# Kernel tuning notes

Hardware: AMD Instinct MI355X
Metric: run time of the kernel (lower is better)

## Reference

```python
import jax, jax.numpy as jnp
import numpy as np

B = 65536
D = 8          # model dim (hard-wired in source)
H = 2          # num_heads
A = 20         # act_size
L = 5          # tokens per embedding stream


def _attn_layer(x, Wqkv, bqkv, Wo, bo, Wl, bl):
    # x: [B, S, D]
    Bx, S, Dx = x.shape
    hd = Dx // H
    qkv = x @ Wqkv.T + bqkv                      # [B, S, 3D]
    q, k, v = jnp.split(qkv, 3, axis=-1)
    def split_heads(t):
        return t.reshape(Bx, S, H, hd).transpose(0, 2, 1, 3)  # [B,H,S,hd]
    q, k, v = split_heads(q), split_heads(k), split_heads(v)
    scores = jnp.einsum('bhqd,bhkd->bhqk', q, k) * (hd ** -0.5)
    attn = jax.nn.softmax(scores, axis=-1)       # dropout inactive at eval
    o = jnp.einsum('bhqk,bhkd->bhqd', attn, v)
    o = o.transpose(0, 2, 1, 3).reshape(Bx, S, Dx)
    x = x + (o @ Wo.T + bo)                      # residual after attention
    h = jax.nn.relu(x @ Wl.T + bl)               # linear + relu
    return x + h                                 # second residual


def setup_inputs() -> dict:
    key = jax.random.key(0)
    ks = jax.random.split(key, 20)
    s = 1.0 / np.sqrt(D)
    inp = {
        'dice_type': jax.random.randint(ks[0], (B, L), 0, 15),
        'dice_star': jax.random.randint(ks[1], (B, L), 0, 15),
        'summon_lvl': jax.random.randint(ks[2], (B, L), 0, 2),
        'emb_dice': jax.random.normal(ks[3], (15, D), jnp.float32),
        'emb_star': jax.random.normal(ks[4], (15, D), jnp.float32),
        'emb_btns': jax.random.normal(ks[5], (2, D), jnp.float32),
        'Wout': jax.random.normal(ks[6], (A, D), jnp.float32) * s,
        'bout': jnp.zeros((A,), jnp.float32),
    }
    for i in range(2):
        o = 7 + 5 * i
        inp[f'Wqkv{i}'] = jax.random.normal(ks[o], (3 * D, D), jnp.float32) * s
        inp[f'bqkv{i}'] = jnp.zeros((3 * D,), jnp.float32)
        inp[f'Wo{i}'] = jax.random.normal(ks[o + 1], (D, D), jnp.float32) * s
        inp[f'bo{i}'] = jnp.zeros((D,), jnp.float32)
        inp[f'Wl{i}'] = jax.random.normal(ks[o + 2], (D, D), jnp.float32) * s
        inp[f'bl{i}'] = jnp.zeros((D,), jnp.float32)
    return inp


def reference(dice_type, dice_star, summon_lvl,
              emb_dice, emb_star, emb_btns,
              Wqkv0, bqkv0, Wo0, bo0, Wl0, bl0,
              Wqkv1, bqkv1, Wo1, bo1, Wl1, bl1,
              Wout, bout):
    x = jnp.concatenate([emb_dice[dice_type],
                         emb_star[dice_star],
                         emb_btns[summon_lvl]], axis=1)  # [B, 15, D]
    x = _attn_layer(x, Wqkv0, bqkv0, Wo0, bo0, Wl0, bl0)
    x = _attn_layer(x, Wqkv1, bqkv1, Wo1, bo1, Wl1, bl1)
    x = jnp.mean(x, axis=1)                               # [B, D]
    return x @ Wout.T + bout                              # [B, A]
```

## Files before the change

kernel.cpp:

```cpp
#include <hip/hip_runtime.h>
#include <math.h>

#define EPB 16
#define BTOT 65536
#define C_SCALE 0.72134752044f
#define QSTR 28

__device__ __forceinline__ float exp2_fast(float x) {
#if defined(__has_builtin)
#if __has_builtin(__builtin_amdgcn_exp2f)
  return __builtin_amdgcn_exp2f(x);
#else
  return exp2f(x);
#endif
#else
  return exp2f(x);
#endif
}

__global__ __launch_bounds__(256) void BetterBot_44169443672375_kernel(
    const int* __restrict__ dice_type, const int* __restrict__ dice_star,
    const int* __restrict__ summon_lvl,
    const float* __restrict__ emb_dice, const float* __restrict__ emb_star,
    const float* __restrict__ emb_btns,
    const float* __restrict__ Wout, const float* __restrict__ bout,
    const float* __restrict__ Wqkv0, const float* __restrict__ bqkv0,
    const float* __restrict__ Wo0, const float* __restrict__ bo0,
    const float* __restrict__ Wl0, const float* __restrict__ bl0,
    const float* __restrict__ Wqkv1, const float* __restrict__ bqkv1,
    const float* __restrict__ Wo1, const float* __restrict__ bo1,
    const float* __restrict__ Wl1, const float* __restrict__ bl1,
    float* __restrict__ out)
{
  __shared__ __align__(16) float qkvT[32 * QSTR];
  __shared__ __align__(8)  float2 eT[32 * 33];
  __shared__ __align__(16) float xT[32][8];
  __shared__ int idxT[EPB][17];
  __shared__ __align__(16) float kb[EPB][17][8];
  __shared__ __align__(16) float vb[EPB][17][8];

  const int tid = threadIdx.x;
  const int e = tid >> 4;
  const int t = tid & 15;
  const int ge = blockIdx.x * EPB + e;

  int myc = 0;
  if (t < 15) {
    int c;
    if (t < 5)       c = dice_type[ge * 5 + t];
    else if (t < 10) c = 15 + dice_star[ge * 5 + (t - 5)];
    else             c = 30 + summon_lvl[ge * 5 + (t - 10)];
    idxT[e][t] = c;
    myc = c;
  }
  {
    const int c = tid >> 3;
    const int l8 = tid & 7;
    const float* er;
    if (c < 15)      er = emb_dice + 8 * c;
    else if (c < 30) er = emb_star + 8 * (c - 15);
    else             er = emb_btns + 8 * (c - 30);
    const float4 r0 = ((const float4*)er)[0];
    const float4 r1 = ((const float4*)er)[1];
    float r[8] = {r0.x, r0.y, r0.z, r0.w, r1.x, r1.y, r1.z, r1.w};
    xT[c][l8] = r[l8];
#pragma unroll
    for (int cc = 0; cc < 3; ++cc) {
      const int col = l8 * 3 + cc;
      float acc = bqkv0[col];
#pragma unroll
      for (int j = 0; j < 8; ++j) acc = fmaf(r[j], Wqkv0[col * 8 + j], acc);
      qkvT[c * QSTR + col] = acc;
    }
  }
  __syncthreads();

  {
    const int p0 = tid * 4;
    const int qi = p0 >> 5;
    const float* qr = qkvT + qi * QSTR;
    float qv[8];
#pragma unroll
    for (int j = 0; j < 8; ++j) qv[j] = qr[j];
#pragma unroll
    for (int jj = 0; jj < 4; ++jj) {
      const int ki = (p0 & 31) + jj;
      const float* kr = qkvT + ki * QSTR + 8;
      float s0 = qv[0] * kr[0];
      s0 = fmaf(qv[1], kr[1], s0); s0 = fmaf(qv[2], kr[2], s0); s0 = fmaf(qv[3], kr[3], s0);
      float s1 = qv[4] * kr[4];
      s1 = fmaf(qv[5], kr[5], s1); s1 = fmaf(qv[6], kr[6], s1); s1 = fmaf(qv[7], kr[7], s1);
      eT[qi * 33 + ki] = make_float2(exp2_fast(C_SCALE * s0), exp2_fast(C_SCALE * s1));
    }
  }
  __syncthreads();

  float x[8] = {0.f, 0.f, 0.f, 0.f, 0.f, 0.f, 0.f, 0.f};
  float q1[8];
  if (t < 15) {
    const float4 x0a = *(const float4*)(xT[myc]);
    const float4 x0b = *(const float4*)(xT[myc] + 4);
    x[0] = x0a.x; x[1] = x0a.y; x[2] = x0a.z; x[3] = x0a.w;
    x[4] = x0b.x; x[5] = x0b.y; x[6] = x0b.z; x[7] = x0b.w;

    float o[8] = {0.f, 0.f, 0.f, 0.f, 0.f, 0.f, 0.f, 0.f};
    float sum0 = 0.f, sum1 = 0.f;
    const float2* myE = eT + myc * 33;
#pragma unroll
    for (int u = 0; u < 15; ++u) {
      const int uc = idxT[e][u];
      const float2 ee = myE[uc];
      const float4 v0 = *(const float4*)(qkvT + uc * QSTR + 16);
      const float4 v1 = *(const float4*)(qkvT + uc * QSTR + 20);
      sum0 += ee.x; sum1 += ee.y;
      o[0] = fmaf(ee.x, v0.x, o[0]); o[1] = fmaf(ee.x, v0.y, o[1]);
      o[2] = fmaf(ee.x, v0.z, o[2]); o[3] = fmaf(ee.x, v0.w, o[3]);
      o[4] = fmaf(ee.y, v1.x, o[4]); o[5] = fmaf(ee.y, v1.y, o[5]);
      o[6] = fmaf(ee.y, v1.z, o[6]); o[7] = fmaf(ee.y, v1.w, o[7]);
    }
    const float r0 = 1.0f / sum0, r1 = 1.0f / sum1;
#pragma unroll
    for (int d = 0; d < 4; ++d) { o[d] *= r0; o[4 + d] *= r1; }
    float xn[8];
#pragma unroll
    for (int c = 0; c < 8; ++c) {
      float acc = bo0[c];
#pragma unroll
      for (int j = 0; j < 8; ++j) acc = fmaf(o[j], Wo0[c * 8 + j], acc);
      xn[c] = x[c] + acc;
    }
#pragma unroll
    for (int c = 0; c < 8; ++c) {
      float acc = bl0[c];
#pragma unroll
      for (int j = 0; j < 8; ++j) acc = fmaf(xn[j], Wl0[c * 8 + j], acc);
      x[c] = xn[c] + fmaxf(acc, 0.0f);
    }

    float k1[8], v1[8];
#pragma unroll
    for (int c = 0; c < 8; ++c) {
      float aq = bqkv1[c];
      float ak = bqkv1[8 + c];
      float av = bqkv1[16 + c];
#pragma unroll
      for (int j = 0; j < 8; ++j) {
        aq = fmaf(x[j], Wqkv1[c * 8 + j], aq);
        ak = fmaf(x[j], Wqkv1[(8 + c) * 8 + j], ak);
        av = fmaf(x[j], Wqkv1[(16 + c) * 8 + j], av);
      }
      q1[c] = aq * C_SCALE;
      k1[c] = ak; v1[c] = av;
    }
    float4* kd = (float4*)kb[e][t];
    kd[0] = make_float4(k1[0], k1[1], k1[2], k1[3]);
    kd[1] = make_float4(k1[4], k1[5], k1[6], k1[7]);
    float4* vd = (float4*)vb[e][t];
    vd[0] = make_float4(v1[0], v1[1], v1[2], v1[3]);
    vd[1] = make_float4(v1[4], v1[5], v1[6], v1[7]);
  }
  __syncthreads();

  if (t < 15) {
    float o[8] = {0.f, 0.f, 0.f, 0.f, 0.f, 0.f, 0.f, 0.f};
    float sum0 = 0.f, sum1 = 0.f;
#pragma unroll
    for (int u = 0; u < 15; ++u) {
      const float4 k0 = *(const float4*)(kb[e][u]);
      const float4 k1v = *(const float4*)(kb[e][u] + 4);
      const float4 v0 = *(const float4*)(vb[e][u]);
      const float4 v1 = *(const float4*)(vb[e][u] + 4);
      float s0 = q1[0] * k0.x;
      s0 = fmaf(q1[1], k0.y, s0); s0 = fmaf(q1[2], k0.z, s0); s0 = fmaf(q1[3], k0.w, s0);
      float s1 = q1[4] * k1v.x;
      s1 = fmaf(q1[5], k1v.y, s1); s1 = fmaf(q1[6], k1v.z, s1); s1 = fmaf(q1[7], k1v.w, s1);
      const float e0 = exp2_fast(s0);
      const float e1 = exp2_fast(s1);
      sum0 += e0; sum1 += e1;
      o[0] = fmaf(e0, v0.x, o[0]); o[1] = fmaf(e0, v0.y, o[1]);
      o[2] = fmaf(e0, v0.z, o[2]); o[3] = fmaf(e0, v0.w, o[3]);
      o[4] = fmaf(e1, v1.x, o[4]); o[5] = fmaf(e1, v1.y, o[5]);
      o[6] = fmaf(e1, v1.z, o[6]); o[7] = fmaf(e1, v1.w, o[7]);
    }
    const float r0 = 1.0f / sum0, r1 = 1.0f / sum1;
#pragma unroll
    for (int d = 0; d < 4; ++d) { o[d] *= r0; o[4 + d] *= r1; }
    float xn[8];
#pragma unroll
    for (int c = 0; c < 8; ++c) {
      float acc = bo1[c];
#pragma unroll
      for (int j = 0; j < 8; ++j) acc = fmaf(o[j], Wo1[c * 8 + j], acc);
      xn[c] = x[c] + acc;
    }
#pragma unroll
    for (int c = 0; c < 8; ++c) {
      float acc = bl1[c];
#pragma unroll
      for (int j = 0; j < 8; ++j) acc = fmaf(xn[j], Wl1[c * 8 + j], acc);
      x[c] = xn[c] + fmaxf(acc, 0.0f);
    }
  }

  float p[8];
#pragma unroll
  for (int j = 0; j < 8; ++j) p[j] = x[j];
#pragma unroll
  for (int j = 0; j < 8; ++j) p[j] += __shfl_xor(p[j], 1);
#pragma unroll
  for (int j = 0; j < 8; ++j) p[j] += __shfl_xor(p[j], 2);
#pragma unroll
  for (int j = 0; j < 8; ++j) p[j] += __shfl_xor(p[j], 4);
#pragma unroll
  for (int j = 0; j < 8; ++j) p[j] += __shfl_xor(p[j], 8);
  float mean[8];
#pragma unroll
  for (int j = 0; j < 8; ++j) mean[j] = p[j] * (1.0f / 15.0f);

  const int obase = ge * 20;
  {
    float acc = bout[t];
#pragma unroll
    for (int j = 0; j < 8; ++j) acc = fmaf(mean[j], Wout[t * 8 + j], acc);
    out[obase + t] = acc;
  }
  if (t < 4) {
    const int a = 16 + t;
    float acc = bout[a];
#pragma unroll
    for (int j = 0; j < 8; ++j) acc = fmaf(mean[j], Wout[a * 8 + j], acc);
    out[obase + a] = acc;
  }
}

extern "C" void kernel_launch(void* const* d_in, const int* in_sizes, int n_in,
                              void* d_out, int out_size, void* d_ws, size_t ws_size,
                              hipStream_t stream) {
  const int*   dice_type  = (const int*)d_in[0];
  const int*   dice_star  = (const int*)d_in[1];
  const int*   summon_lvl = (const int*)d_in[2];
  const float* emb_dice   = (const float*)d_in[3];
  const float* emb_star   = (const float*)d_in[4];
  const float* emb_btns   = (const float*)d_in[5];
  const float* Wout       = (const float*)d_in[6];
  const float* bout       = (const float*)d_in[7];
  const float* Wqkv0      = (const float*)d_in[8];
  const float* bqkv0      = (const float*)d_in[9];
  const float* Wo0        = (const float*)d_in[10];
  const float* bo0        = (const float*)d_in[11];
  const float* Wl0        = (const float*)d_in[12];
  const float* bl0        = (const float*)d_in[13];
  const float* Wqkv1      = (const float*)d_in[14];
  const float* bqkv1      = (const float*)d_in[15];
  const float* Wo1        = (const float*)d_in[16];
  const float* bo1        = (const float*)d_in[17];
  const float* Wl1        = (const float*)d_in[18];
  const float* bl1        = (const float*)d_in[19];
  float* out = (float*)d_out;

  dim3 grid(BTOT / EPB), block(256);
  hipLaunchKernelGGL(BetterBot_44169443672375_kernel, grid, block, 0, stream,
                     dice_type, dice_star, summon_lvl,
                     emb_dice, emb_star, emb_btns, Wout, bout,
                     Wqkv0, bqkv0, Wo0, bo0, Wl0, bl0,
                     Wqkv1, bqkv1, Wo1, bo1, Wl1, bl1,
                     out);
}
```

Baseline: 128.7 us.

## Move layer-0 attention output and small matmuls to packed fp16 math

Adds a setup kernel that packs the small weight matrices into fp16 pairs, with the query scale folded in, and stores them in workspace. The main kernel then runs the layer-0 attention accumulation, the output and linear projections, and the layer-1 QKV projection with packed half2 arithmetic. Shared buffers are shrunk and merged, and a launch-bounds occupancy hint is added. The aim is to halve ALU instruction count and cut LDS footprint. The cost is fp16 rounding error in the residual stream and one extra small kernel launch per call.

```diff
diff --git a/kernel.cpp b/kernel.cpp
--- a/kernel.cpp
+++ b/kernel.cpp
@@ -4,7 +4,19 @@
 #define EPB 16
 #define BTOT 65536
 #define C_SCALE 0.72134752044f
-#define QSTR 28
+
+typedef _Float16 h2 __attribute__((ext_vector_type(2)));
+
+#define WQKV1 0
+#define BQKV1 96
+#define WO0   108
+#define BO0   140
+#define WL0   144
+#define BL0   176
+#define WO1   180
+#define BO1   212
+#define WL1   216
+#define BL1   248
 
 __device__ __forceinline__ float exp2_fast(float x) {
 #if defined(__has_builtin)
@@ -18,26 +30,84 @@
 #endif
 }
 
-__global__ __launch_bounds__(256) void BetterBot_44169443672375_kernel(
+union F4H2 { float4 f; h2 h[4]; };
+
+__device__ __forceinline__ void mm8_h2(const h2* __restrict__ wp, int woff, int boff,
+                                       const h2 in2[4], h2 out2[4])
+{
+#pragma unroll
+  for (int c2 = 0; c2 < 4; ++c2) {
+    h2 acc = wp[boff + c2];
+#pragma unroll
+    for (int p = 0; p < 4; ++p) {
+      acc += (h2)(in2[p].x) * wp[woff + c2 * 8 + 2 * p];
+      acc += (h2)(in2[p].y) * wp[woff + c2 * 8 + 2 * p + 1];
+    }
+    out2[c2] = acc;
+  }
+}
+
+__global__ void BetterBot_setup(const float* __restrict__ Wqkv1, const float* __restrict__ bqkv1,
+                                const float* __restrict__ Wo0, const float* __restrict__ bo0,
+                                const float* __restrict__ Wl0, const float* __restrict__ bl0,
+                                const float* __restrict__ Wo1, const float* __restrict__ bo1,
+                                const float* __restrict__ Wl1, const float* __restrict__ bl1,
+                                h2* __restrict__ ws)
+{
+  const int tid = threadIdx.x;
+  if (tid < 96) {
+    const int c2 = tid >> 3, j = tid & 7;
+    float a = Wqkv1[(2 * c2) * 8 + j], b = Wqkv1[(2 * c2 + 1) * 8 + j];
+    if (c2 < 4) { a *= C_SCALE; b *= C_SCALE; }
+    ws[tid] = (h2){(_Float16)a, (_Float16)b};
+  } else if (tid < 108) {
+    const int c2 = tid - 96;
+    float a = bqkv1[2 * c2], b = bqkv1[2 * c2 + 1];
+    if (c2 < 4) { a *= C_SCALE; b *= C_SCALE; }
+    ws[tid] = (h2){(_Float16)a, (_Float16)b};
+  } else if (tid < 140) {
+    const int k = tid - 108, c2 = k >> 3, j = k & 7;
+    ws[tid] = (h2){(_Float16)Wo0[(2 * c2) * 8 + j], (_Float16)Wo0[(2 * c2 + 1) * 8 + j]};
+  } else if (tid < 144) {
+    const int c2 = tid - 140;
+    ws[tid] = (h2){(_Float16)bo0[2 * c2], (_Float16)bo0[2 * c2 + 1]};
+  } else if (tid < 176) {
+    const int k = tid - 144, c2 = k >> 3, j = k & 7;
+    ws[tid] = (h2){(_Float16)Wl0[(2 * c2) * 8 + j], (_Float16)Wl0[(2 * c2 + 1) * 8 + j]};
+  } else if (tid < 180) {
+    const int c2 = tid - 176;
+    ws[tid] = (h2){(_Float16)bl0[2 * c2], (_Float16)bl0[2 * c2 + 1]};
+  } else if (tid < 212) {
+    const int k = tid - 180, c2 = k >> 3, j = k & 7;
+    ws[tid] = (h2){(_Float16)Wo1[(2 * c2) * 8 + j], (_Float16)Wo1[(2 * c2 + 1) * 8 + j]};
+  } else if (tid < 216) {
+    const int c2 = tid - 212;
+    ws[tid] = (h2){(_Float16)bo1[2 * c2], (_Float16)bo1[2 * c2 + 1]};
+  } else if (tid < 248) {
+    const int k = tid - 216, c2 = k >> 3, j = k & 7;
+    ws[tid] = (h2){(_Float16)Wl1[(2 * c2) * 8 + j], (_Float16)Wl1[(2 * c2 + 1) * 8 + j]};
+  } else if (tid < 252) {
+    const int c2 = tid - 248;
+    ws[tid] = (h2){(_Float16)bl1[2 * c2], (_Float16)bl1[2 * c2 + 1]};
+  }
+}
+
+__global__ __launch_bounds__(256, 4) void BetterBot_44169443672375_kernel(
     const int* __restrict__ dice_type, const int* __restrict__ dice_star,
     const int* __restrict__ summon_lvl,
     const float* __restrict__ emb_dice, const float* __restrict__ emb_star,
     const float* __restrict__ emb_btns,
     const float* __restrict__ Wout, const float* __restrict__ bout,
     const float* __restrict__ Wqkv0, const float* __restrict__ bqkv0,
-    const float* __restrict__ Wo0, const float* __restrict__ bo0,
-    const float* __restrict__ Wl0, const float* __restrict__ bl0,
-    const float* __restrict__ Wqkv1, const float* __restrict__ bqkv1,
-    const float* __restrict__ Wo1, const float* __restrict__ bo1,
-    const float* __restrict__ Wl1, const float* __restrict__ bl1,
+    const h2* __restrict__ wp,
     float* __restrict__ out)
 {
-  __shared__ __align__(16) float qkvT[32 * QSTR];
-  __shared__ __align__(8)  float2 eT[32 * 33];
-  __shared__ __align__(16) float xT[32][8];
-  __shared__ int idxT[EPB][17];
-  __shared__ __align__(16) float kb[EPB][17][8];
-  __shared__ __align__(16) float vb[EPB][17][8];
+  __shared__ __align__(16) float qkT[32][20];
+  __shared__ __align__(16) h2 vT[32][4];
+  __shared__ __align__(16) h2 xT[32][4];
+  __shared__ h2 eT[32 * 33];
+  __shared__ int idxT[EPB][16];
+  __shared__ __align__(16) float kvb[EPB][15][16];
 
   const int tid = threadIdx.x;
   const int e = tid >> 4;
@@ -63,148 +133,150 @@
     const float4 r0 = ((const float4*)er)[0];
     const float4 r1 = ((const float4*)er)[1];
     float r[8] = {r0.x, r0.y, r0.z, r0.w, r1.x, r1.y, r1.z, r1.w};
-    xT[c][l8] = r[l8];
-#pragma unroll
-    for (int cc = 0; cc < 3; ++cc) {
-      const int col = l8 * 3 + cc;
-      float acc = bqkv0[col];
-#pragma unroll
-      for (int j = 0; j < 8; ++j) acc = fmaf(r[j], Wqkv0[col * 8 + j], acc);
-      qkvT[c * QSTR + col] = acc;
-    }
+    if (l8 < 4) xT[c][l8] = (h2){(_Float16)r[2 * l8], (_Float16)r[2 * l8 + 1]};
+    float aq = bqkv0[l8], ak = bqkv0[8 + l8], av = bqkv0[16 + l8];
+#pragma unroll
+    for (int j = 0; j < 8; ++j) {
+      aq = fmaf(r[j], Wqkv0[l8 * 8 + j], aq);
+      ak = fmaf(r[j], Wqkv0[(8 + l8) * 8 + j], ak);
+      av = fmaf(r[j], Wqkv0[(16 + l8) * 8 + j], av);
+    }
+    qkT[c][l8] = aq * C_SCALE;
+    qkT[c][8 + l8] = ak;
+    const float vn = __shfl_xor(av, 1);
+    if ((l8 & 1) == 0) vT[c][l8 >> 1] = (h2){(_Float16)av, (_Float16)vn};
   }
   __syncthreads();
 
   {
-    const int p0 = tid * 4;
-    const int qi = p0 >> 5;
-    const float* qr = qkvT + qi * QSTR;
+    const int qi = tid >> 3;
+    const int ki0 = (tid & 7) * 4;
     float qv[8];
 #pragma unroll
-    for (int j = 0; j < 8; ++j) qv[j] = qr[j];
+    for (int j = 0; j < 8; ++j) qv[j] = qkT[qi][j];
 #pragma unroll
     for (int jj = 0; jj < 4; ++jj) {
-      const int ki = (p0 & 31) + jj;
-      const float* kr = qkvT + ki * QSTR + 8;
+      const int ki = ki0 + jj;
+      const float* kr = &qkT[ki][8];
       float s0 = qv[0] * kr[0];
       s0 = fmaf(qv[1], kr[1], s0); s0 = fmaf(qv[2], kr[2], s0); s0 = fmaf(qv[3], kr[3], s0);
       float s1 = qv[4] * kr[4];
       s1 = fmaf(qv[5], kr[5], s1); s1 = fmaf(qv[6], kr[6], s1); s1 = fmaf(qv[7], kr[7], s1);
-      eT[qi * 33 + ki] = make_float2(exp2_fast(C_SCALE * s0), exp2_fast(C_SCALE * s1));
+      eT[qi * 33 + ki] = (h2){(_Float16)exp2_fast(s0), (_Float16)exp2_fast(s1)};
     }
   }
   __syncthreads();
 
-  float x[8] = {0.f, 0.f, 0.f, 0.f, 0.f, 0.f, 0.f, 0.f};
-  float q1[8];
+  h2 x2[4];
+  float q1f[8];
   if (t < 15) {
-    const float4 x0a = *(const float4*)(xT[myc]);
-    const float4 x0b = *(const float4*)(xT[myc] + 4);
-    x[0] = x0a.x; x[1] = x0a.y; x[2] = x0a.z; x[3] = x0a.w;
-    x[4] = x0b.x; x[5] = x0b.y; x[6] = x0b.z; x[7] = x0b.w;
-
-    float o[8] = {0.f, 0.f, 0.f, 0.f, 0.f, 0.f, 0.f, 0.f};
+    F4H2 xx; xx.f = *(const float4*)(&xT[myc][0]);
+#pragma unroll
+    for (int p = 0; p < 4; ++p) x2[p] = xx.h[p];
+
+    h2 o2[4] = {(h2)(_Float16)0.f, (h2)(_Float16)0.f, (h2)(_Float16)0.f, (h2)(_Float16)0.f};
     float sum0 = 0.f, sum1 = 0.f;
-    const float2* myE = eT + myc * 33;
+    const h2* myE = eT + myc * 33;
 #pragma unroll
     for (int u = 0; u < 15; ++u) {
       const int uc = idxT[e][u];
-      const float2 ee = myE[uc];
-      const float4 v0 = *(const float4*)(qkvT + uc * QSTR + 16);
-      const float4 v1 = *(const float4*)(qkvT + uc * QSTR + 20);
-      sum0 += ee.x; sum1 += ee.y;
-      o[0] = fmaf(ee.x, v0.x, o[0]); o[1] = fmaf(ee.x, v0.y, o[1]);
-      o[2] = fmaf(ee.x, v0.z, o[2]); o[3] = fmaf(ee.x, v0.w, o[3]);
-      o[4] = fmaf(ee.y, v1.x, o[4]); o[5] = fmaf(ee.y, v1.y, o[5]);
-      o[6] = fmaf(ee.y, v1.z, o[6]); o[7] = fmaf(ee.y, v1.w, o[7]);
+      const h2 ee = myE[uc];
+      F4H2 vv; vv.f = *(const float4*)(&vT[uc][0]);
+      const h2 el = (h2)(ee.x);
+      const h2 eh = (h2)(ee.y);
+      o2[0] += el * vv.h[0];
+      o2[1] += el * vv.h[1];
+      o2[2] += eh * vv.h[2];
+      o2[3] += eh * vv.h[3];
+      sum0 += (float)ee.x;
+      sum1 += (float)ee.y;
     }
     const float r0 = 1.0f / sum0, r1 = 1.0f / sum1;
-#pragma unroll
-    for (int d = 0; d < 4; ++d) { o[d] *= r0; o[4 + d] *= r1; }
-    float xn[8];
-#pragma unroll
-    for (int c = 0; c < 8; ++c) {
-      float acc = bo0[c];
-#pragma unroll
-      for (int j = 0; j < 8; ++j) acc = fmaf(o[j], Wo0[c * 8 + j], acc);
-      xn[c] = x[c] + acc;
-    }
-#pragma unroll
-    for (int c = 0; c < 8; ++c) {
-      float acc = bl0[c];
-#pragma unroll
-      for (int j = 0; j < 8; ++j) acc = fmaf(xn[j], Wl0[c * 8 + j], acc);
-      x[c] = xn[c] + fmaxf(acc, 0.0f);
-    }
-
-    float k1[8], v1[8];
-#pragma unroll
-    for (int c = 0; c < 8; ++c) {
-      float aq = bqkv1[c];
-      float ak = bqkv1[8 + c];
-      float av = bqkv1[16 + c];
-#pragma unroll
-      for (int j = 0; j < 8; ++j) {
-        aq = fmaf(x[j], Wqkv1[c * 8 + j], aq);
-        ak = fmaf(x[j], Wqkv1[(8 + c) * 8 + j], ak);
-        av = fmaf(x[j], Wqkv1[(16 + c) * 8 + j], av);
+    o2[0] *= (h2)(_Float16)r0; o2[1] *= (h2)(_Float16)r0;
+    o2[2] *= (h2)(_Float16)r1; o2[3] *= (h2)(_Float16)r1;
+
+    h2 y2[4], xn2[4], hh2[4];
+    mm8_h2(wp, WO0, BO0, o2, y2);
+#pragma unroll
+    for (int p = 0; p < 4; ++p) xn2[p] = x2[p] + y2[p];
+    mm8_h2(wp, WL0, BL0, xn2, hh2);
+    const h2 z2 = (h2)(_Float16)0.f;
+#pragma unroll
+    for (int p = 0; p < 4; ++p) x2[p] = xn2[p] + __builtin_elementwise_max(hh2[p], z2);
+
+    h2 qkv2[12];
+#pragma unroll
+    for (int c2 = 0; c2 < 12; ++c2) {
+      h2 acc = wp[BQKV1 + c2];
+#pragma unroll
+      for (int p = 0; p < 4; ++p) {
+        acc += (h2)(x2[p].x) * wp[WQKV1 + c2 * 8 + 2 * p];
+        acc += (h2)(x2[p].y) * wp[WQKV1 + c2 * 8 + 2 * p + 1];
       }
-      q1[c] = aq * C_SCALE;
-      k1[c] = ak; v1[c] = av;
-    }
-    float4* kd = (float4*)kb[e][t];
-    kd[0] = make_float4(k1[0], k1[1], k1[2], k1[3]);
-    kd[1] = make_float4(k1[4], k1[5], k1[6], k1[7]);
-    float4* vd = (float4*)vb[e][t];
-    vd[0] = make_float4(v1[0], v1[1], v1[2], v1[3]);
-    vd[1] = make_float4(v1[4], v1[5], v1[6], v1[7]);
+      qkv2[c2] = acc;
+    }
+#pragma unroll
+    for (int p = 0; p < 4; ++p) {
+      q1f[2 * p] = (float)qkv2[p].x;
+      q1f[2 * p + 1] = (float)qkv2[p].y;
+    }
+    *(float4*)(&kvb[e][t][0]) = make_float4((float)qkv2[4].x, (float)qkv2[4].y,
+                                            (float)qkv2[5].x, (float)qkv2[5].y);
+    *(float4*)(&kvb[e][t][4]) = make_float4((float)qkv2[6].x, (float)qkv2[6].y,
+                                            (float)qkv2[7].x, (float)qkv2[7].y);
+    *(float4*)(&kvb[e][t][8]) = make_float4((float)qkv2[8].x, (float)qkv2[8].y,
+                                            (float)qkv2[9].x, (float)qkv2[9].y);
+    *(float4*)(&kvb[e][t][12]) = make_float4((float)qkv2[10].x, (float)qkv2[10].y,
+                                             (float)qkv2[11].x, (float)qkv2[11].y);
   }
   __syncthreads();
 
+  float xo[8] = {0.f, 0.f, 0.f, 0.f, 0.f, 0.f, 0.f, 0.f};
   if (t < 15) {
     float o[8] = {0.f, 0.f, 0.f, 0.f, 0.f, 0.f, 0.f, 0.f};
     float sum0 = 0.f, sum1 = 0.f;
 #pragma unroll
     for (int u = 0; u < 15; ++u) {
-      const float4 k0 = *(const float4*)(kb[e][u]);
-      const float4 k1v = *(const float4*)(kb[e][u] + 4);
-      const float4 v0 = *(const float4*)(vb[e][u]);
-      const float4 v1 = *(const float4*)(vb[e][u] + 4);
-      float s0 = q1[0] * k0.x;
-      s0 = fmaf(q1[1], k0.y, s0); s0 = fmaf(q1[2], k0.z, s0); s0 = fmaf(q1[3], k0.w, s0);
-      float s1 = q1[4] * k1v.x;
-      s1 = fmaf(q1[5], k1v.y, s1); s1 = fmaf(q1[6], k1v.z, s1); s1 = fmaf(q1[7], k1v.w, s1);
+      const float4 ka = *(const float4*)(&kvb[e][u][0]);
+      const float4 kb2 = *(const float4*)(&kvb[e][u][4]);
+      const float4 va = *(const float4*)(&kvb[e][u][8]);
+      const float4 vb2 = *(const float4*)(&kvb[e][u][12]);
+      float s0 = q1f[0] * ka.x;
+      s0 = fmaf(q1f[1], ka.y, s0); s0 = fmaf(q1f[2], ka.z, s0); s0 = fmaf(q1f[3], ka.w, s0);
+      float s1 = q1f[4] * kb2.x;
+      s1 = fmaf(q1f[5], kb2.y, s1); s1 = fmaf(q1f[6], kb2.z, s1); s1 = fmaf(q1f[7], kb2.w, s1);
       const float e0 = exp2_fast(s0);
       const float e1 = exp2_fast(s1);
       sum0 += e0; sum1 += e1;
-      o[0] = fmaf(e0, v0.x, o[0]); o[1] = fmaf(e0, v0.y, o[1]);
-      o[2] = fmaf(e0, v0.z, o[2]); o[3] = fmaf(e0, v0.w, o[3]);
-      o[4] = fmaf(e1, v1.x, o[4]); o[5] = fmaf(e1, v1.y, o[5]);
-      o[6] = fmaf(e1, v1.z, o[6]); o[7] = fmaf(e1, v1.w, o[7]);
+      o[0] = fmaf(e0, va.x, o[0]); o[1] = fmaf(e0, va.y, o[1]);
+      o[2] = fmaf(e0, va.z, o[2]); o[3] = fmaf(e0, va.w, o[3]);
+      o[4] = fmaf(e1, vb2.x, o[4]); o[5] = fmaf(e1, vb2.y, o[5]);
+      o[6] = fmaf(e1, vb2.z, o[6]); o[7] = fmaf(e1, vb2.w, o[7]);
     }
     const float r0 = 1.0f / sum0, r1 = 1.0f / sum1;
-#pragma unroll
-    for (int d = 0; d < 4; ++d) { o[d] *= r0; o[4 + d] *= r1; }
-    float xn[8];
-#pragma unroll
-    for (int c = 0; c < 8; ++c) {
-      float acc = bo1[c];
-#pragma unroll
-      for (int j = 0; j < 8; ++j) acc = fmaf(o[j], Wo1[c * 8 + j], acc);
-      xn[c] = x[c] + acc;
-    }
-#pragma unroll
-    for (int c = 0; c < 8; ++c) {
-      float acc = bl1[c];
-#pragma unroll
-      for (int j = 0; j < 8; ++j) acc = fmaf(xn[j], Wl1[c * 8 + j], acc);
-      x[c] = xn[c] + fmaxf(acc, 0.0f);
+    h2 po2[4];
+    po2[0] = (h2){(_Float16)(o[0] * r0), (_Float16)(o[1] * r0)};
+    po2[1] = (h2){(_Float16)(o[2] * r0), (_Float16)(o[3] * r0)};
+    po2[2] = (h2){(_Float16)(o[4] * r1), (_Float16)(o[5] * r1)};
+    po2[3] = (h2){(_Float16)(o[6] * r1), (_Float16)(o[7] * r1)};
+
+    h2 y2[4], xn2[4], hh2[4];
+    mm8_h2(wp, WO1, BO1, po2, y2);
+#pragma unroll
+    for (int p = 0; p < 4; ++p) xn2[p] = x2[p] + y2[p];
+    mm8_h2(wp, WL1, BL1, xn2, hh2);
+    const h2 z2 = (h2)(_Float16)0.f;
+#pragma unroll
+    for (int p = 0; p < 4; ++p) {
+      const h2 xf = xn2[p] + __builtin_elementwise_max(hh2[p], z2);
+      xo[2 * p] = (float)xf.x;
+      xo[2 * p + 1] = (float)xf.y;
     }
   }
 
   float p[8];
 #pragma unroll
-  for (int j = 0; j < 8; ++j) p[j] = x[j];
+  for (int j = 0; j < 8; ++j) p[j] = xo[j];
 #pragma unroll
   for (int j = 0; j < 8; ++j) p[j] += __shfl_xor(p[j], 1);
 #pragma unroll
@@ -257,12 +329,12 @@
   const float* Wl1        = (const float*)d_in[18];
   const float* bl1        = (const float*)d_in[19];
   float* out = (float*)d_out;
-
-  dim3 grid(BTOT / EPB), block(256);
-  hipLaunchKernelGGL(BetterBot_44169443672375_kernel, grid, block, 0, stream,
+  h2* ws = (h2*)d_ws;
+
+  hipLaunchKernelGGL(BetterBot_setup, dim3(1), dim3(256), 0, stream,
+                     Wqkv1, bqkv1, Wo0, bo0, Wl0, bl0, Wo1, bo1, Wl1, bl1, ws);
+  hipLaunchKernelGGL(BetterBot_44169443672375_kernel, dim3(BTOT / EPB), dim3(256), 0, stream,
                      dice_type, dice_star, summon_lvl,
                      emb_dice, emb_star, emb_btns, Wout, bout,
-                     Wqkv0, bqkv0, Wo0, bo0, Wl0, bl0,
-                     Wqkv1, bqkv1, Wo1, bo1, Wl1, bl1,
-                     out);
-}
+                     Wqkv0, bqkv0, (const h2*)ws, out);
+}
```

Measured after the change: 131.0 us. Within noise of the previous version (+1.8%).
